# Kernel optimization log

Measured on AMD Instinct MI355X. Metric: run time of the kernel, lower is better.

## Reference

```python
import jax, jax.numpy as jnp
import numpy as np

N = 100000      # nodes
E = 1600000     # edges (avg degree 16)
IN = 128        # in_channels
OUT = 64        # out_channels
HID = 2 * OUT   # hidden = 2*out_channels


def setup_inputs() -> dict:
    key = jax.random.key(0)
    ks = jax.random.split(key, 9)
    x = jax.random.normal(ks[0], (N, IN), jnp.float32)
    edge_index = jax.random.randint(ks[1], (2, E), 0, N, jnp.int32)
    init_dist = jax.random.normal(ks[2], (N, OUT), jnp.float32)
    # GCNConv weights (glorot-ish scale) and biases
    W1 = jax.random.normal(ks[3], (IN, HID), jnp.float32) * (1.0 / np.sqrt(IN))
    b1 = jnp.zeros((HID,), jnp.float32)
    Wmu = jax.random.normal(ks[4], (HID, OUT), jnp.float32) * (1.0 / np.sqrt(HID))
    bmu = jnp.zeros((OUT,), jnp.float32)
    Wls = jax.random.normal(ks[5], (HID, OUT), jnp.float32) * (1.0 / np.sqrt(HID))
    bls = jnp.zeros((OUT,), jnp.float32)
    return {"x": x, "edge_index": edge_index, "init_dist": init_dist,
            "W1": W1, "b1": b1, "Wmu": Wmu, "bmu": bmu, "Wls": Wls, "bls": bls}


def _gcn(h, src, dst, norm, W, b, n):
    # dense transform, then normalized scatter-add aggregation over edges
    h = h @ W                               # [N, F]
    msg = h[src] * norm[:, None]            # gather + scale  [E', F]
    out = jax.ops.segment_sum(msg, dst, num_segments=n)
    return out + b


def reference(x, edge_index, init_dist, W1, b1, Wmu, bmu, Wls, bls):
    n = x.shape[0]
    # add self-loops (PyG GCNConv default)
    loops = jnp.arange(n, dtype=edge_index.dtype)
    src = jnp.concatenate([edge_index[0], loops])
    dst = jnp.concatenate([edge_index[1], loops])
    # symmetric normalization: deg over A+I, norm_e = d_src^-1/2 * d_dst^-1/2
    deg = jax.ops.segment_sum(jnp.ones_like(dst, dtype=x.dtype), dst, num_segments=n)
    dinv = jax.lax.rsqrt(jnp.maximum(deg, 1.0))  # deg >= 1 thanks to self-loops
    norm = dinv[src] * dinv[dst]

    h = _gcn(x, src, dst, norm, W1, b1, n)       # conv1 (no activation in source)
    mu = _gcn(h, src, dst, norm, Wmu, bmu, n)
    logstd = _gcn(h, src, dst, norm, Wls, bls, n)
    # reparametrize: mu + init_dist * exp(logstd)
    return mu + init_dist * jnp.exp(logstd)
```

## Files before the change

kernel.cpp:

```cpp
#include <hip/hip_runtime.h>
#include <math.h>

#define NN 100000
#define NE 1600000
#define SLOTS 48
#define NODES_PER_BUCKET 12500
#define QUADS (NE / 4)
#define CSEG 128
#define QPS2 ((QUADS + CSEG - 1) / CSEG)
#define XCAST_T (NN * 32)
#define PREP_T (XCAST_T + 16384 + 128)
#define PREP_B ((PREP_T + 255) / 256)
#define FRONT_B (1024 + PREP_B)

__device__ __forceinline__ float bf2f(unsigned int u) {
    union { unsigned int u; float f; } c; c.u = u << 16; return c.f;
}
__device__ __forceinline__ unsigned short f2bf(float f) {
    union { float f; unsigned int u; } c; c.f = f;
    unsigned int x = c.u;
    return (unsigned short)((x + 0x7fffu + ((x >> 16) & 1u)) >> 16);
}

typedef __attribute__((ext_vector_type(8))) short short8;
typedef __attribute__((ext_vector_type(4))) float float4v;

__global__ __launch_bounds__(256) void k_front(const int* __restrict__ ei,
        int* __restrict__ cnt, int* __restrict__ csr48,
        const float* __restrict__ x, unsigned short* __restrict__ xq,
        const float* __restrict__ W1, const float* __restrict__ Wmu,
        const float* __restrict__ Wls, const float* __restrict__ b1,
        unsigned short* __restrict__ W2c, float* __restrict__ bw) {
    int b = blockIdx.x;
    if (b < 1024) {
        int bucket = b & 7;
        int seg = b >> 3;
        int lo = bucket * NODES_PER_BUCKET, hi = lo + NODES_PER_BUCKET;
        int q1 = min((seg + 1) * QPS2, QUADS);
        for (int q = seg * QPS2 + (int)threadIdx.x; q < q1; q += 256) {
            int e0 = q * 4;
            int4 s = *(const int4*)(ei + e0);
            int4 d = *(const int4*)(ei + NE + e0);
            int r;
            if (d.x >= lo && d.x < hi) { r = atomicAdd(&cnt[d.x], 1); if (r < SLOTS) csr48[d.x * SLOTS + r] = s.x; }
            if (d.y >= lo && d.y < hi) { r = atomicAdd(&cnt[d.y], 1); if (r < SLOTS) csr48[d.y * SLOTS + r] = s.y; }
            if (d.z >= lo && d.z < hi) { r = atomicAdd(&cnt[d.z], 1); if (r < SLOTS) csr48[d.z * SLOTS + r] = s.z; }
            if (d.w >= lo && d.w < hi) { r = atomicAdd(&cnt[d.w], 1); if (r < SLOTS) csr48[d.w * SLOTS + r] = s.w; }
        }
    } else {
        int idx = (b - 1024) * 256 + (int)threadIdx.x;
        if (idx < XCAST_T) {
            int node = idx >> 5, c = (idx & 31) << 2;
            float4 v = *(const float4*)(x + (size_t)node * 128 + c);
            uint2 st;
            st.x = ((unsigned int)f2bf(v.y) << 16) | f2bf(v.x);
            st.y = ((unsigned int)f2bf(v.w) << 16) | f2bf(v.z);
            *(uint2*)(xq + (size_t)node * 128 + c) = st;
        } else if (idx < XCAST_T + 16384) {
            int j = idx - XCAST_T;
            int k = j >> 7, n = j & 127;
            const float* Wx = (n < 64) ? (Wmu + n) : (Wls + (n - 64));
            float s = 0.f;
#pragma unroll 8
            for (int m = 0; m < 128; ++m) s += W1[k * 128 + m] * Wx[(size_t)m * 64];
            W2c[n * 128 + k] = f2bf(s);
        } else if (idx < PREP_T) {
            int n = idx - XCAST_T - 16384;
            const float* Wx = (n < 64) ? (Wmu + n) : (Wls + (n - 64));
            float s = 0.f;
            for (int m = 0; m < 128; ++m) s += b1[m] * Wx[(size_t)m * 64];
            bw[n] = s;
        }
    }
}

__global__ __launch_bounds__(256) void k_gather1(
    const unsigned short* __restrict__ tab, const int* __restrict__ cnt,
    const int* __restrict__ csr48,
    unsigned short* __restrict__ yout, float* __restrict__ avec) {
    int node = blockIdx.x * 4 + (threadIdx.x >> 6);
    int lane = threadIdx.x & 63;
    int q = lane >> 4, l16 = lane & 15;
    int deg = __builtin_amdgcn_readfirstlane(cnt[node]);
    float dn = rsqrtf((float)(deg + 1));
    if (deg > SLOTS) deg = SLOTS;
    float a[8] = {0.f, 0.f, 0.f, 0.f, 0.f, 0.f, 0.f, 0.f};
    float asum = 0.f;
    if (q == 0) {
        uint4 p = *(const uint4*)(tab + (size_t)node * 128 + l16 * 8);
        a[0] = dn * bf2f(p.x & 0xffffu); a[1] = dn * bf2f(p.x >> 16);
        a[2] = dn * bf2f(p.y & 0xffffu); a[3] = dn * bf2f(p.y >> 16);
        a[4] = dn * bf2f(p.z & 0xffffu); a[5] = dn * bf2f(p.z >> 16);
        a[6] = dn * bf2f(p.w & 0xffffu); a[7] = dn * bf2f(p.w >> 16);
    }
    int base = node * SLOTS;
    int t = q;
    while (t + 4 < deg) {
        int s0 = csr48[base + t];
        int s1 = csr48[base + t + 4];
        float d0 = rsqrtf((float)(cnt[s0] + 1));
        float d1 = rsqrtf((float)(cnt[s1] + 1));
        uint4 r0 = *(const uint4*)(tab + (size_t)s0 * 128 + l16 * 8);
        uint4 r1 = *(const uint4*)(tab + (size_t)s1 * 128 + l16 * 8);
        asum += d0 + d1;
        a[0] += d0 * bf2f(r0.x & 0xffffu) + d1 * bf2f(r1.x & 0xffffu);
        a[1] += d0 * bf2f(r0.x >> 16)     + d1 * bf2f(r1.x >> 16);
        a[2] += d0 * bf2f(r0.y & 0xffffu) + d1 * bf2f(r1.y & 0xffffu);
        a[3] += d0 * bf2f(r0.y >> 16)     + d1 * bf2f(r1.y >> 16);
        a[4] += d0 * bf2f(r0.z & 0xffffu) + d1 * bf2f(r1.z & 0xffffu);
        a[5] += d0 * bf2f(r0.z >> 16)     + d1 * bf2f(r1.z >> 16);
        a[6] += d0 * bf2f(r0.w & 0xffffu) + d1 * bf2f(r1.w & 0xffffu);
        a[7] += d0 * bf2f(r0.w >> 16)     + d1 * bf2f(r1.w >> 16);
        t += 8;
    }
    while (t < deg) {
        int s = csr48[base + t];
        float ds = rsqrtf((float)(cnt[s] + 1));
        uint4 r = *(const uint4*)(tab + (size_t)s * 128 + l16 * 8);
        asum += ds;
        a[0] += ds * bf2f(r.x & 0xffffu); a[1] += ds * bf2f(r.x >> 16);
        a[2] += ds * bf2f(r.y & 0xffffu); a[3] += ds * bf2f(r.y >> 16);
        a[4] += ds * bf2f(r.z & 0xffffu); a[5] += ds * bf2f(r.z >> 16);
        a[6] += ds * bf2f(r.w & 0xffffu); a[7] += ds * bf2f(r.w >> 16);
        t += 4;
    }
#pragma unroll
    for (int j = 0; j < 8; ++j) {
        a[j] += __shfl_xor(a[j], 16);
        a[j] += __shfl_xor(a[j], 32);
    }
    asum += __shfl_xor(asum, 16);
    asum += __shfl_xor(asum, 32);
    if (q == 0) {
        float d2 = dn * dn;
        uint4 st;
        st.x = ((unsigned int)f2bf(a[1] * d2) << 16) | f2bf(a[0] * d2);
        st.y = ((unsigned int)f2bf(a[3] * d2) << 16) | f2bf(a[2] * d2);
        st.z = ((unsigned int)f2bf(a[5] * d2) << 16) | f2bf(a[4] * d2);
        st.w = ((unsigned int)f2bf(a[7] * d2) << 16) | f2bf(a[6] * d2);
        *(uint4*)(yout + (size_t)node * 128 + l16 * 8) = st;
        if (l16 == 0) avec[node] = dn * (asum + dn);
    }
}

__global__ __launch_bounds__(256) void k_gather2(
    const unsigned short* __restrict__ tab, const int* __restrict__ cnt,
    const int* __restrict__ csr48, unsigned short* __restrict__ yout) {
    int node = blockIdx.x * 4 + (threadIdx.x >> 6);
    int lane = threadIdx.x & 63;
    int q = lane >> 4, l16 = lane & 15;
    int deg = __builtin_amdgcn_readfirstlane(cnt[node]);
    float dn = rsqrtf((float)(deg + 1));
    if (deg > SLOTS) deg = SLOTS;
    float a[8] = {0.f, 0.f, 0.f, 0.f, 0.f, 0.f, 0.f, 0.f};
    if (q == 0) {
        uint4 p = *(const uint4*)(tab + (size_t)node * 128 + l16 * 8);
        a[0] = bf2f(p.x & 0xffffu); a[1] = bf2f(p.x >> 16);
        a[2] = bf2f(p.y & 0xffffu); a[3] = bf2f(p.y >> 16);
        a[4] = bf2f(p.z & 0xffffu); a[5] = bf2f(p.z >> 16);
        a[6] = bf2f(p.w & 0xffffu); a[7] = bf2f(p.w >> 16);
    }
    int base = node * SLOTS;
    int t = q;
    while (t + 4 < deg) {
        int s0 = csr48[base + t];
        int s1 = csr48[base + t + 4];
        uint4 r0 = *(const uint4*)(tab + (size_t)s0 * 128 + l16 * 8);
        uint4 r1 = *(const uint4*)(tab + (size_t)s1 * 128 + l16 * 8);
        a[0] += bf2f(r0.x & 0xffffu) + bf2f(r1.x & 0xffffu);
        a[1] += bf2f(r0.x >> 16)     + bf2f(r1.x >> 16);
        a[2] += bf2f(r0.y & 0xffffu) + bf2f(r1.y & 0xffffu);
        a[3] += bf2f(r0.y >> 16)     + bf2f(r1.y >> 16);
        a[4] += bf2f(r0.z & 0xffffu) + bf2f(r1.z & 0xffffu);
        a[5] += bf2f(r0.z >> 16)     + bf2f(r1.z >> 16);
        a[6] += bf2f(r0.w & 0xffffu) + bf2f(r1.w & 0xffffu);
        a[7] += bf2f(r0.w >> 16)     + bf2f(r1.w >> 16);
        t += 8;
    }
    while (t < deg) {
        int s = csr48[base + t];
        uint4 r = *(const uint4*)(tab + (size_t)s * 128 + l16 * 8);
        a[0] += bf2f(r.x & 0xffffu); a[1] += bf2f(r.x >> 16);
        a[2] += bf2f(r.y & 0xffffu); a[3] += bf2f(r.y >> 16);
        a[4] += bf2f(r.z & 0xffffu); a[5] += bf2f(r.z >> 16);
        a[6] += bf2f(r.w & 0xffffu); a[7] += bf2f(r.w >> 16);
        t += 4;
    }
#pragma unroll
    for (int j = 0; j < 8; ++j) {
        a[j] += __shfl_xor(a[j], 16);
        a[j] += __shfl_xor(a[j], 32);
    }
    if (q == 0) {
        uint4 st;
        st.x = ((unsigned int)f2bf(a[1] * dn) << 16) | f2bf(a[0] * dn);
        st.y = ((unsigned int)f2bf(a[3] * dn) << 16) | f2bf(a[2] * dn);
        st.z = ((unsigned int)f2bf(a[5] * dn) << 16) | f2bf(a[4] * dn);
        st.w = ((unsigned int)f2bf(a[7] * dn) << 16) | f2bf(a[6] * dn);
        *(uint4*)(yout + (size_t)node * 128 + l16 * 8) = st;
    }
}

__global__ __launch_bounds__(256) void k_gemmC(
    const unsigned short* __restrict__ g2,
    const unsigned short* __restrict__ Bt,
    const float* __restrict__ bw,
    const float* __restrict__ avec,
    const float* __restrict__ bmu,
    const float* __restrict__ bls,
    const float* __restrict__ init,
    float* __restrict__ outp,
    int nrows) {
    __shared__ __align__(16) unsigned short As[64 * 136];
    int tid = threadIdx.x;
    int r0 = blockIdx.x * 64;
    for (int c = tid; c < 1024; c += 256) {
        int row = c >> 4, kc = (c & 15) << 3;
        int gr = r0 + row;
        short8 v = {0, 0, 0, 0, 0, 0, 0, 0};
        if (gr < nrows) v = *(const short8*)(g2 + (size_t)gr * 128 + kc);
        *(short8*)(As + row * 136 + kc) = v;
    }
    __syncthreads();
    int lane = tid & 63, wave = tid >> 6;
    int quad = lane >> 4, l16 = lane & 15;
    int cm = wave * 16 + l16;
    int cl = 64 + cm;
    float4v acc[4][2];
#pragma unroll
    for (int rt = 0; rt < 4; ++rt) {
        float4v z = {0.f, 0.f, 0.f, 0.f};
        acc[rt][0] = z; acc[rt][1] = z;
    }
#pragma unroll
    for (int ks = 0; ks < 4; ++ks) {
        short8 b0 = *(const short8*)(Bt + (size_t)cm * 128 + ks * 32 + quad * 8);
        short8 b1 = *(const short8*)(Bt + (size_t)cl * 128 + ks * 32 + quad * 8);
        short8 af[4];
#pragma unroll
        for (int rt = 0; rt < 4; ++rt)
            af[rt] = *(const short8*)(As + (rt * 16 + l16) * 136 + ks * 32 + quad * 8);
#pragma unroll
        for (int rt = 0; rt < 4; ++rt) {
            acc[rt][0] = __builtin_amdgcn_mfma_f32_16x16x32_bf16(af[rt], b0, acc[rt][0], 0, 0, 0);
            acc[rt][1] = __builtin_amdgcn_mfma_f32_16x16x32_bf16(af[rt], b1, acc[rt][1], 0, 0, 0);
        }
    }
    float bc_mu = bmu[cm], bc_ls = bls[cm];
    float bwm = bw[cm], bwl = bw[cl];
#pragma unroll
    for (int rt = 0; rt < 4; ++rt)
#pragma unroll
        for (int reg = 0; reg < 4; ++reg) {
            int gr = r0 + rt * 16 + quad * 4 + reg;
            if (gr < nrows) {
                float av = avec[gr];
                float mu = acc[rt][0][reg] + av * bwm + bc_mu;
                float ls = acc[rt][1][reg] + av * bwl + bc_ls;
                float idv = init[(size_t)gr * 64 + cm];
                outp[(size_t)gr * 64 + cm] = mu + idv * expf(ls);
            }
        }
}

extern "C" void kernel_launch(void* const* d_in, const int* in_sizes, int n_in,
                              void* d_out, int out_size, void* d_ws, size_t ws_size,
                              hipStream_t stream) {
    const float* x   = (const float*)d_in[0];
    const int*   ei  = (const int*)d_in[1];
    const float* ind = (const float*)d_in[2];
    const float* W1  = (const float*)d_in[3];
    const float* b1  = (const float*)d_in[4];
    const float* Wmu = (const float*)d_in[5];
    const float* bmu = (const float*)d_in[6];
    const float* Wls = (const float*)d_in[7];
    const float* bls = (const float*)d_in[8];
    float* outp = (float*)d_out;

    char* w = (char*)d_ws;
    auto carve = [&](size_t bytes) -> char* {
        char* p = w; w += (bytes + 255) & ~(size_t)255; return p;
    };
    int*   cnt  = (int*)carve((size_t)NN * 4);
    float* avec = (float*)carve((size_t)NN * 4);
    float* bw   = (float*)carve(128 * 4);
    unsigned short* W2c = (unsigned short*)carve(128 * 128 * 2);
    unsigned short* xs  = (unsigned short*)carve((size_t)NN * 128 * 2);
    unsigned short* t1  = (unsigned short*)carve((size_t)NN * 128 * 2);
    int* csr = (int*)carve((size_t)NN * SLOTS * 4);

    hipMemsetAsync(cnt, 0, (size_t)NN * 4, stream);
    k_front<<<FRONT_B, 256, 0, stream>>>(ei, cnt, csr, x, xs, W1, Wmu, Wls, b1, W2c, bw);
    k_gather1<<<NN / 4, 256, 0, stream>>>(xs, cnt, csr, t1, avec);
    k_gather2<<<NN / 4, 256, 0, stream>>>(t1, cnt, csr, xs);
    k_gemmC<<<(NN + 63) / 64, 256, 0, stream>>>(xs, W2c, bw, avec, bmu, bls, ind, outp, NN);
}
```

Measured before the change: 356.0 us.

## Fuse second gather with output GEMM and reparametrize epilogue

Merges the second aggregation kernel with the final projection kernel. Each wave keeps its aggregated node row in shared memory as fp32 and computes the 64 mu and logstd outputs with a scalar per-lane dot product over 128 bf16 weights. This removes the bf16 round trip of the intermediate buffer and one kernel launch. In exchange it drops the MFMA tiles for scalar FMAs, and the W2c weight rows are read with strided per-lane accesses, which may raise memory or ALU cost.

```diff
diff --git a/kernel.cpp b/kernel.cpp
--- a/kernel.cpp
+++ b/kernel.cpp
@@ -21,9 +21,6 @@
     unsigned int x = c.u;
     return (unsigned short)((x + 0x7fffu + ((x >> 16) & 1u)) >> 16);
 }
-
-typedef __attribute__((ext_vector_type(8))) short short8;
-typedef __attribute__((ext_vector_type(4))) float float4v;
 
 __global__ __launch_bounds__(256) void k_front(const int* __restrict__ ei,
         int* __restrict__ cnt, int* __restrict__ csr48,
@@ -143,11 +140,20 @@
     }
 }
 
-__global__ __launch_bounds__(256) void k_gather2(
-    const unsigned short* __restrict__ tab, const int* __restrict__ cnt,
-    const int* __restrict__ csr48, unsigned short* __restrict__ yout) {
-    int node = blockIdx.x * 4 + (threadIdx.x >> 6);
-    int lane = threadIdx.x & 63;
+__global__ __launch_bounds__(256) void k_gather2C(
+    const unsigned short* __restrict__ tab,
+    const int* __restrict__ cnt, const int* __restrict__ csr48,
+    const unsigned short* __restrict__ W2c,
+    const float* __restrict__ bw,
+    const float* __restrict__ avec,
+    const float* __restrict__ bmu, const float* __restrict__ bls,
+    const float* __restrict__ init,
+    float* __restrict__ outp) {
+    __shared__ float rowbuf[4][132];
+    int tid = threadIdx.x;
+    int n4 = tid >> 6;
+    int node = blockIdx.x * 4 + n4;
+    int lane = tid & 63;
     int q = lane >> 4, l16 = lane & 15;
     int deg = __builtin_amdgcn_readfirstlane(cnt[node]);
     float dn = rsqrtf((float)(deg + 1));
@@ -192,75 +198,26 @@
         a[j] += __shfl_xor(a[j], 32);
     }
     if (q == 0) {
-        uint4 st;
-        st.x = ((unsigned int)f2bf(a[1] * dn) << 16) | f2bf(a[0] * dn);
-        st.y = ((unsigned int)f2bf(a[3] * dn) << 16) | f2bf(a[2] * dn);
-        st.z = ((unsigned int)f2bf(a[5] * dn) << 16) | f2bf(a[4] * dn);
-        st.w = ((unsigned int)f2bf(a[7] * dn) << 16) | f2bf(a[6] * dn);
-        *(uint4*)(yout + (size_t)node * 128 + l16 * 8) = st;
-    }
-}
-
-__global__ __launch_bounds__(256) void k_gemmC(
-    const unsigned short* __restrict__ g2,
-    const unsigned short* __restrict__ Bt,
-    const float* __restrict__ bw,
-    const float* __restrict__ avec,
-    const float* __restrict__ bmu,
-    const float* __restrict__ bls,
-    const float* __restrict__ init,
-    float* __restrict__ outp,
-    int nrows) {
-    __shared__ __align__(16) unsigned short As[64 * 136];
-    int tid = threadIdx.x;
-    int r0 = blockIdx.x * 64;
-    for (int c = tid; c < 1024; c += 256) {
-        int row = c >> 4, kc = (c & 15) << 3;
-        int gr = r0 + row;
-        short8 v = {0, 0, 0, 0, 0, 0, 0, 0};
-        if (gr < nrows) v = *(const short8*)(g2 + (size_t)gr * 128 + kc);
-        *(short8*)(As + row * 136 + kc) = v;
+#pragma unroll
+        for (int j = 0; j < 8; ++j) rowbuf[n4][l16 * 8 + j] = a[j] * dn;
     }
     __syncthreads();
-    int lane = tid & 63, wave = tid >> 6;
-    int quad = lane >> 4, l16 = lane & 15;
-    int cm = wave * 16 + l16;
-    int cl = 64 + cm;
-    float4v acc[4][2];
-#pragma unroll
-    for (int rt = 0; rt < 4; ++rt) {
-        float4v z = {0.f, 0.f, 0.f, 0.f};
-        acc[rt][0] = z; acc[rt][1] = z;
-    }
-#pragma unroll
-    for (int ks = 0; ks < 4; ++ks) {
-        short8 b0 = *(const short8*)(Bt + (size_t)cm * 128 + ks * 32 + quad * 8);
-        short8 b1 = *(const short8*)(Bt + (size_t)cl * 128 + ks * 32 + quad * 8);
-        short8 af[4];
-#pragma unroll
-        for (int rt = 0; rt < 4; ++rt)
-            af[rt] = *(const short8*)(As + (rt * 16 + l16) * 136 + ks * 32 + quad * 8);
-#pragma unroll
-        for (int rt = 0; rt < 4; ++rt) {
-            acc[rt][0] = __builtin_amdgcn_mfma_f32_16x16x32_bf16(af[rt], b0, acc[rt][0], 0, 0, 0);
-            acc[rt][1] = __builtin_amdgcn_mfma_f32_16x16x32_bf16(af[rt], b1, acc[rt][1], 0, 0, 0);
-        }
-    }
-    float bc_mu = bmu[cm], bc_ls = bls[cm];
-    float bwm = bw[cm], bwl = bw[cl];
-#pragma unroll
-    for (int rt = 0; rt < 4; ++rt)
-#pragma unroll
-        for (int reg = 0; reg < 4; ++reg) {
-            int gr = r0 + rt * 16 + quad * 4 + reg;
-            if (gr < nrows) {
-                float av = avec[gr];
-                float mu = acc[rt][0][reg] + av * bwm + bc_mu;
-                float ls = acc[rt][1][reg] + av * bwl + bc_ls;
-                float idv = init[(size_t)gr * 64 + cm];
-                outp[(size_t)gr * 64 + cm] = mu + idv * expf(ls);
-            }
-        }
+    int cm = lane;
+    const float* row = rowbuf[n4];
+    const unsigned short* wm = W2c + (size_t)cm * 128;
+    const unsigned short* wl = W2c + (size_t)(cm + 64) * 128;
+    float accm = 0.f, accl = 0.f;
+#pragma unroll 16
+    for (int k = 0; k < 128; ++k) {
+        float rk = row[k];
+        accm += rk * bf2f(wm[k]);
+        accl += rk * bf2f(wl[k]);
+    }
+    float av = avec[node];
+    float mu = accm + av * bw[cm] + bmu[cm];
+    float ls = accl + av * bw[cm + 64] + bls[cm];
+    float idv = init[(size_t)node * 64 + cm];
+    outp[(size_t)node * 64 + cm] = mu + idv * expf(ls);
 }
 
 extern "C" void kernel_launch(void* const* d_in, const int* in_sizes, int n_in,
@@ -292,6 +249,5 @@
     hipMemsetAsync(cnt, 0, (size_t)NN * 4, stream);
     k_front<<<FRONT_B, 256, 0, stream>>>(ei, cnt, csr, x, xs, W1, Wmu, Wls, b1, W2c, bw);
     k_gather1<<<NN / 4, 256, 0, stream>>>(xs, cnt, csr, t1, avec);
-    k_gather2<<<NN / 4, 256, 0, stream>>>(t1, cnt, csr, xs);
-    k_gemmC<<<(NN + 63) / 64, 256, 0, stream>>>(xs, W2c, bw, avec, bmu, bls, ind, outp, NN);
-}
+    k_gather2C<<<NN / 4, 256, 0, stream>>>(t1, cnt, csr, W2c, bw, avec, bmu, bls, ind, outp);
+}
```

New measurement: 655.9 us. 84.2% more time.
